# Kernel tuning notes

Hardware: AMD Instinct MI355X
Metric: run time of the kernel (lower is better)

The kernel has to match this reference:

```python
import jax, jax.numpy as jnp
import numpy as np

CNT_R = 500
DIM = 128
B, NEI = 8192, 64


def setup_inputs() -> dict:
    key = jax.random.key(0)
    ks = jax.random.split(key, 10)
    d2 = 2 * DIM
    return {
        "batch_nei_e_emb": jax.random.normal(ks[0], (B, NEI, DIM), dtype=jnp.float32),
        "batch_nei_rw": jax.random.uniform(ks[1], (B, NEI), dtype=jnp.float32),
        "w_r_table": jax.random.normal(ks[2], (2 * CNT_R + 1, DIM), dtype=jnp.float32),
        "zq_table": jax.random.normal(ks[3], (2 * CNT_R, DIM), dtype=jnp.float32),
        "attn_W_w": jax.random.normal(ks[4], (d2, d2), dtype=jnp.float32) / np.sqrt(d2),
        "attn_W_b": jnp.zeros((d2,), dtype=jnp.float32),
        "u_a_w": jax.random.normal(ks[5], (d2,), dtype=jnp.float32) / np.sqrt(d2),
        "u_a_b": jnp.zeros((), dtype=jnp.float32),
        "batch_nei_rid": jax.random.randint(ks[6], (B, NEI), 0, 2 * CNT_R + 1),
        "batch_q_rid": jax.random.randint(ks[7], (B,), 0, 2 * CNT_R),
    }


def reference(batch_nei_e_emb, batch_nei_rw, w_r_table, zq_table,
              attn_W_w, attn_W_b, u_a_w, u_a_b,
              batch_nei_rid, batch_q_rid):
    # gather relation hyperplane normals: (B, NEI, DIM)
    w_r = w_r_table[batch_nei_rid]
    n = w_r / jnp.linalg.norm(w_r, axis=-1, keepdims=True)
    # hyperplane projection: e - (e . n) n
    e = batch_nei_e_emb
    e_proj = e - jnp.sum(e * n, axis=-1, keepdims=True) * n
    # query relation embedding, tiled over neighbors: (B, NEI, DIM)
    z_q = zq_table[batch_q_rid]  # (B, DIM)
    z_q = jnp.broadcast_to(z_q[:, None, :], e_proj.shape)
    concat = jnp.concatenate([z_q, e_proj], axis=-1)  # (B, NEI, 2*DIM)
    h = jnp.tanh(jnp.einsum('bni,oi->bno', concat, attn_W_w) + attn_W_b)
    _alpha = jnp.einsum('bni,i->bn', h, u_a_w) + u_a_b  # (B, NEI)
    alpha = jax.nn.softmax(_alpha, axis=-1)
    attn = alpha + batch_nei_rw
    return attn
```

## Files before the change

### kernel.cpp

```cpp
#include <hip/hip_runtime.h>

#define NB    8192
#define NEI   64
#define DIM   128
#define D2    256
#define NR_W  1001
#define NR_Z  1000
#define EPB_LD 136

typedef __attribute__((ext_vector_type(8))) short bf16x8;
typedef __attribute__((ext_vector_type(4))) float f32x4;

__device__ __forceinline__ ushort f2bf(float x) {
    union { float f; unsigned u; } c; c.f = x;
    unsigned u = c.u;
    return (ushort)((u + 0x7fffu + ((u >> 16) & 1u)) >> 16);
}


__global__ void k_norm(const float* __restrict__ w_r_table, float* __restrict__ norm_t) {
    int r = blockIdx.x;
    int t = threadIdx.x;
    float v = w_r_table[r * DIM + t];
    float s = v * v;
    #pragma unroll
    for (int m = 1; m < 64; m <<= 1) s += __shfl_xor(s, m);
    __shared__ float sh[2];
    if ((t & 63) == 0) sh[t >> 6] = s;
    __syncthreads();
    float tot = sh[0] + sh[1];
    norm_t[r * DIM + t] = v / sqrtf(tot);
}

__global__ void k_tq(const float* __restrict__ zq_table, const float* __restrict__ W,
                     const float* __restrict__ bias, float* __restrict__ tq_t) {
    int r = blockIdx.x;
    int o = threadIdx.x;
    __shared__ float4 z4[32];
    if (o < 32) z4[o] = ((const float4*)(zq_table + r * DIM))[o];
    __syncthreads();
    const float4* wr = (const float4*)(W + o * D2);
    float acc = bias[o];
    #pragma unroll 8
    for (int i = 0; i < 32; ++i) {
        float4 wv = wr[i], zv = z4[i];
        acc += wv.x*zv.x + wv.y*zv.y + wv.z*zv.z + wv.w*zv.w;
    }
    tq_t[r * D2 + o] = acc;
}

__global__ void k_bfrag(const float* __restrict__ W, ushort* __restrict__ bfrag) {
    int nt = blockIdx.x;
    int kt = blockIdx.y;
    int l  = threadIdx.x;
    int o  = nt * 16 + (l & 15);
    int k  = kt * 32 + (l >> 4) * 8;
    const float4* src = (const float4*)(W + o * D2 + DIM + k);
    float4 a = src[0], c = src[1];
    uint4 w;
    w.x = f2bf(a.x) | ((unsigned)f2bf(a.y) << 16);
    w.y = f2bf(a.z) | ((unsigned)f2bf(a.w) << 16);
    w.z = f2bf(c.x) | ((unsigned)f2bf(c.y) << 16);
    w.w = f2bf(c.z) | ((unsigned)f2bf(c.w) << 16);
    *(uint4*)(bfrag + ((nt * 4 + kt) * 64 + l) * 8) = w;
}


__global__ __launch_bounds__(256, 2) void k_main(
    const float* __restrict__ e_emb,
    const float* __restrict__ rw,
    const int*   __restrict__ nei_rid,
    const int*   __restrict__ q_rid,
    const float* __restrict__ norm_t,
    const float* __restrict__ tq_t,
    const ushort* __restrict__ bfrag,
    const float* __restrict__ u_a_w,
    float* __restrict__ out)
{
    __shared__ ushort ep16[NEI * EPB_LD];
    __shared__ float  alpw[4][NEI];

    const int b = blockIdx.x;
    const int t = threadIdx.x;
    const int wave = t >> 6, lane = t & 63;
    const int ln = lane & 15, hi = lane >> 4;

    {
        const int row = t >> 2, q = t & 3;
        const float4* esrc = (const float4*)(e_emb + ((size_t)b * NEI + row) * DIM + q * 32);
        const int rid = nei_rid[b * NEI + row];
        const float4* nsrc = (const float4*)(norm_t + rid * DIM + q * 32);
        float4 ev[8], nv[8];
        #pragma unroll
        for (int i = 0; i < 8; ++i) { ev[i] = esrc[i]; nv[i] = nsrc[i]; }
        float part = 0.f;
        #pragma unroll
        for (int i = 0; i < 8; ++i)
            part += ev[i].x*nv[i].x + ev[i].y*nv[i].y + ev[i].z*nv[i].z + ev[i].w*nv[i].w;
        part += __shfl_xor(part, 1);
        part += __shfl_xor(part, 2);
        const float d = part;
        ushort* dst = &ep16[row * EPB_LD + q * 32];
        #pragma unroll
        for (int g = 0; g < 4; ++g) {
            float4 lo = ev[g*2], hi4 = ev[g*2+1];
            float4 nl = nv[g*2], nh  = nv[g*2+1];
            lo.x = fmaf(-d, nl.x, lo.x); lo.y = fmaf(-d, nl.y, lo.y);
            lo.z = fmaf(-d, nl.z, lo.z); lo.w = fmaf(-d, nl.w, lo.w);
            hi4.x = fmaf(-d, nh.x, hi4.x); hi4.y = fmaf(-d, nh.y, hi4.y);
            hi4.z = fmaf(-d, nh.z, hi4.z); hi4.w = fmaf(-d, nh.w, hi4.w);
            uint4 w;
            w.x = f2bf(lo.x)  | ((unsigned)f2bf(lo.y)  << 16);
            w.y = f2bf(lo.z)  | ((unsigned)f2bf(lo.w)  << 16);
            w.z = f2bf(hi4.x) | ((unsigned)f2bf(hi4.y) << 16);
            w.w = f2bf(hi4.z) | ((unsigned)f2bf(hi4.w) << 16);
            *(uint4*)(dst + g * 8) = w;
        }
    }

    const int qr = q_rid[b];
    float tq4[4], ua4[4];
    #pragma unroll
    for (int nt = 0; nt < 4; ++nt) {
        int o = wave * 64 + nt * 16 + ln;
        tq4[nt] = tq_t[qr * D2 + o];
        ua4[nt] = u_a_w[o];
    }

    bf16x8 bfr_[4][4];
    #pragma unroll
    for (int nt = 0; nt < 4; ++nt)
        #pragma unroll
        for (int kt = 0; kt < 4; ++kt)
            bfr_[nt][kt] = *(const bf16x8*)(bfrag + (((wave*4 + nt)*4 + kt)*64 + lane)*8);

    __syncthreads();

    #pragma unroll
    for (int mt = 0; mt < 4; ++mt) {
        bf16x8 a_[4];
        #pragma unroll
        for (int kt = 0; kt < 4; ++kt)
            a_[kt] = *(const bf16x8*)&ep16[(mt*16 + ln) * EPB_LD + kt*32 + hi*8];
        f32x4 acc[4];
        #pragma unroll
        for (int nt = 0; nt < 4; ++nt) acc[nt] = (f32x4){0.f, 0.f, 0.f, 0.f};
        #pragma unroll
        for (int kt = 0; kt < 4; ++kt)
            #pragma unroll
            for (int nt = 0; nt < 4; ++nt)
                acc[nt] = __builtin_amdgcn_mfma_f32_16x16x32_bf16(a_[kt], bfr_[nt][kt], acc[nt], 0, 0, 0);
        float pr[4] = {0.f, 0.f, 0.f, 0.f};
        #pragma unroll
        for (int nt = 0; nt < 4; ++nt)
            #pragma unroll
            for (int j = 0; j < 4; ++j) {
                float v = acc[nt][j] + tq4[nt];
                float e2 = __expf(2.f * v);
                float r  = __builtin_amdgcn_rcpf(e2 + 1.f);
                float h  = fmaf(-2.f, r, 1.f);
                pr[j] += ua4[nt] * h;
            }
        #pragma unroll
        for (int m = 1; m < 16; m <<= 1)
            #pragma unroll
            for (int j = 0; j < 4; ++j) pr[j] += __shfl_xor(pr[j], m);
        if (ln == 0) {
            #pragma unroll
            for (int j = 0; j < 4; ++j) alpw[wave][mt*16 + hi*4 + j] = pr[j];
        }
    }
    __syncthreads();

    if (t < NEI) {
        float a = alpw[0][t] + alpw[1][t] + alpw[2][t] + alpw[3][t];
        float p = __expf(a);
        float s = p;
        #pragma unroll
        for (int m = 1; m < 64; m <<= 1) s += __shfl_xor(s, m);
        out[(size_t)b * NEI + t] = fmaf(p, __builtin_amdgcn_rcpf(s), rw[(size_t)b * NEI + t]);
    }
}


extern "C" void kernel_launch(void* const* d_in, const int* in_sizes, int n_in,
                              void* d_out, int out_size, void* d_ws, size_t ws_size,
                              hipStream_t stream) {
    const float* e_emb   = (const float*)d_in[0];
    const float* rw      = (const float*)d_in[1];
    const float* w_r_tab = (const float*)d_in[2];
    const float* zq_tab  = (const float*)d_in[3];
    const float* attn_W  = (const float*)d_in[4];
    const float* attn_b  = (const float*)d_in[5];
    const float* u_a_w   = (const float*)d_in[6];
    const int*   nei_rid = (const int*)d_in[8];
    const int*   q_rid   = (const int*)d_in[9];
    float* out = (float*)d_out;

    float* ws = (float*)d_ws;
    float* norm_t = ws;
    float* tq_t   = norm_t + NR_W * DIM;
    ushort* bfrag = (ushort*)(tq_t + NR_Z * D2);

    k_norm<<<NR_W, DIM, 0, stream>>>(w_r_tab, norm_t);
    k_tq<<<NR_Z, D2, 0, stream>>>(zq_tab, attn_W, attn_b, tq_t);
    k_bfrag<<<dim3(16, 4), 64, 0, stream>>>(attn_W, bfrag);
    k_main<<<NB, 256, 0, stream>>>(e_emb, rw, nei_rid, q_rid,
                                   norm_t, tq_t, bfrag, u_a_w, out);
}
```

Baseline: 126.9 us.

## Make main kernel persistent over 16 batches with async LDS prefetch of embeddings

Each workgroup now runs 512 threads and loops over 16 batch rows. The next row's embedding tile is prefetched straight into LDS with global_load_lds, and its rid/rw/tq values are loaded into registers while the current row computes. B fragments are loaded once per block and split across 8 waves. The tanh is rewritten algebraically as 1-2/(1+exp2) with the u_a sum precomputed, which saves a multiply per element. This aims to hide HBM latency and amortise setup, at the cost of more LDS, an extra barrier per row and fewer blocks (512).

```diff
diff --git a/kernel.cpp b/kernel.cpp
--- a/kernel.cpp
+++ b/kernel.cpp
@@ -1,4 +1,5 @@
 #include <hip/hip_runtime.h>
+#include <hip/hip_bf16.h>
 
 #define NB    8192
 #define NEI   64
@@ -7,6 +8,8 @@
 #define NR_W  1001
 #define NR_Z  1000
 #define EPB_LD 136
+#define BPB   16
+#define C2L2E 2.8853900817779268f
 
 typedef __attribute__((ext_vector_type(8))) short bf16x8;
 typedef __attribute__((ext_vector_type(4))) float f32x4;
@@ -15,6 +18,17 @@
     union { float f; unsigned u; } c; c.f = x;
     unsigned u = c.u;
     return (ushort)((u + 0x7fffu + ((u >> 16) & 1u)) >> 16);
+}
+
+__device__ __forceinline__ unsigned pk2(float a, float b) {
+    __hip_bfloat162 h = __float22bfloat162_rn(make_float2(a, b));
+    return *(unsigned*)&h;
+}
+
+__device__ __forceinline__ void gll16(const void* g, void* l) {
+    __builtin_amdgcn_global_load_lds(
+        (const __attribute__((address_space(1))) unsigned int*)g,
+        (__attribute__((address_space(3))) unsigned int*)l, 16, 0, 0);
 }
 
 
@@ -50,10 +64,10 @@
 }
 
 __global__ void k_bfrag(const float* __restrict__ W, ushort* __restrict__ bfrag) {
-    int nt = blockIdx.x;
+    int ot = blockIdx.x;
     int kt = blockIdx.y;
     int l  = threadIdx.x;
-    int o  = nt * 16 + (l & 15);
+    int o  = ot * 16 + (l & 15);
     int k  = kt * 32 + (l >> 4) * 8;
     const float4* src = (const float4*)(W + o * D2 + DIM + k);
     float4 a = src[0], c = src[1];
@@ -62,11 +76,22 @@
     w.y = f2bf(a.z) | ((unsigned)f2bf(a.w) << 16);
     w.z = f2bf(c.x) | ((unsigned)f2bf(c.y) << 16);
     w.w = f2bf(c.z) | ((unsigned)f2bf(c.w) << 16);
-    *(uint4*)(bfrag + ((nt * 4 + kt) * 64 + l) * 8) = w;
-}
-
-
-__global__ __launch_bounds__(256, 2) void k_main(
+    *(uint4*)(bfrag + ((ot * 4 + kt) * 64 + l) * 8) = w;
+}
+
+__global__ void k_sua(const float* __restrict__ u, float* __restrict__ sua) {
+    int t = threadIdx.x;
+    float v = u[t];
+    #pragma unroll
+    for (int m = 1; m < 64; m <<= 1) v += __shfl_xor(v, m);
+    __shared__ float sh[4];
+    if ((t & 63) == 0) sh[t >> 6] = v;
+    __syncthreads();
+    if (t == 0) sua[0] = sh[0] + sh[1] + sh[2] + sh[3];
+}
+
+
+__global__ __launch_bounds__(512, 4) void k_main(
     const float* __restrict__ e_emb,
     const float* __restrict__ rw,
     const int*   __restrict__ nei_rid,
@@ -74,111 +99,167 @@
     const float* __restrict__ norm_t,
     const float* __restrict__ tq_t,
     const ushort* __restrict__ bfrag,
+    const float* __restrict__ u_a_sum,
     const float* __restrict__ u_a_w,
     float* __restrict__ out)
 {
-    __shared__ ushort ep16[NEI * EPB_LD];
-    __shared__ float  alpw[4][NEI];
-
-    const int b = blockIdx.x;
-    const int t = threadIdx.x;
+    __shared__ __align__(16) float  e_raw[NEI * DIM];
+    __shared__ __align__(16) ushort ep16[NEI * EPB_LD];
+    __shared__ float alpw[8][NEI];
+
+    const int t    = threadIdx.x;
     const int wave = t >> 6, lane = t & 63;
-    const int ln = lane & 15, hi = lane >> 4;
-
-    {
-        const int row = t >> 2, q = t & 3;
-        const float4* esrc = (const float4*)(e_emb + ((size_t)b * NEI + row) * DIM + q * 32);
-        const int rid = nei_rid[b * NEI + row];
-        const float4* nsrc = (const float4*)(norm_t + rid * DIM + q * 32);
-        float4 ev[8], nv[8];
-        #pragma unroll
-        for (int i = 0; i < 8; ++i) { ev[i] = esrc[i]; nv[i] = nsrc[i]; }
-        float part = 0.f;
-        #pragma unroll
-        for (int i = 0; i < 8; ++i)
-            part += ev[i].x*nv[i].x + ev[i].y*nv[i].y + ev[i].z*nv[i].z + ev[i].w*nv[i].w;
-        part += __shfl_xor(part, 1);
-        part += __shfl_xor(part, 2);
-        const float d = part;
-        ushort* dst = &ep16[row * EPB_LD + q * 32];
-        #pragma unroll
-        for (int g = 0; g < 4; ++g) {
-            float4 lo = ev[g*2], hi4 = ev[g*2+1];
-            float4 nl = nv[g*2], nh  = nv[g*2+1];
-            lo.x = fmaf(-d, nl.x, lo.x); lo.y = fmaf(-d, nl.y, lo.y);
-            lo.z = fmaf(-d, nl.z, lo.z); lo.w = fmaf(-d, nl.w, lo.w);
-            hi4.x = fmaf(-d, nh.x, hi4.x); hi4.y = fmaf(-d, nh.y, hi4.y);
-            hi4.z = fmaf(-d, nh.z, hi4.z); hi4.w = fmaf(-d, nh.w, hi4.w);
-            uint4 w;
-            w.x = f2bf(lo.x)  | ((unsigned)f2bf(lo.y)  << 16);
-            w.y = f2bf(lo.z)  | ((unsigned)f2bf(lo.w)  << 16);
-            w.z = f2bf(hi4.x) | ((unsigned)f2bf(hi4.y) << 16);
-            w.w = f2bf(hi4.z) | ((unsigned)f2bf(hi4.w) << 16);
-            *(uint4*)(dst + g * 8) = w;
-        }
-    }
-
-    const int qr = q_rid[b];
-    float tq4[4], ua4[4];
-    #pragma unroll
-    for (int nt = 0; nt < 4; ++nt) {
-        int o = wave * 64 + nt * 16 + ln;
-        tq4[nt] = tq_t[qr * D2 + o];
-        ua4[nt] = u_a_w[o];
-    }
-
-    bf16x8 bfr_[4][4];
-    #pragma unroll
-    for (int nt = 0; nt < 4; ++nt)
+    const int ln   = lane & 15, hi = lane >> 4;
+    const int row  = t >> 3, q3 = t & 7;
+    const int b0   = blockIdx.x * BPB;
+
+    bf16x8 bfr_[2][4];
+    #pragma unroll
+    for (int nt = 0; nt < 2; ++nt)
         #pragma unroll
         for (int kt = 0; kt < 4; ++kt)
-            bfr_[nt][kt] = *(const bf16x8*)(bfrag + (((wave*4 + nt)*4 + kt)*64 + lane)*8);
-
-    __syncthreads();
-
-    #pragma unroll
-    for (int mt = 0; mt < 4; ++mt) {
-        bf16x8 a_[4];
+            bfr_[nt][kt] = *(const bf16x8*)(bfrag + ((((wave*2+nt)*4 + kt)*64 + lane)*8));
+    asm volatile("" : "+v"(bfr_[0][0]), "+v"(bfr_[0][1]), "+v"(bfr_[0][2]), "+v"(bfr_[0][3]),
+                      "+v"(bfr_[1][0]), "+v"(bfr_[1][1]), "+v"(bfr_[1][2]), "+v"(bfr_[1][3]));
+
+    float ua2[2];
+    #pragma unroll
+    for (int nt = 0; nt < 2; ++nt) ua2[nt] = u_a_w[wave*32 + nt*16 + ln];
+    asm volatile("" : "+v"(ua2[0]), "+v"(ua2[1]));
+    const float sua = u_a_sum[0];
+
+    unsigned soff[4];
+    #pragma unroll
+    for (int c = 0; c < 4; ++c) {
+        unsigned D = (unsigned)(wave*4096 + c*1024 + lane*16);
+        unsigned r7 = (unsigned)((wave*8 + 2*c + (lane>>5)) & 7);
+        soff[c] = D ^ (r7 << 4);
+    }
+    const char* ebase = (const char*)e_emb;
+
+    #pragma unroll
+    for (int c = 0; c < 4; ++c)
+        gll16(ebase + (((size_t)b0) << 15) + soff[c], (char*)e_raw + wave*4096 + c*1024);
+    int   rid_c = nei_rid[b0 * NEI + row];
+    float rw_c  = rw[(size_t)b0 * NEI + (t & 63)];
+    float tqc[2];
+    {
+        int qr = q_rid[b0];
         #pragma unroll
-        for (int kt = 0; kt < 4; ++kt)
-            a_[kt] = *(const bf16x8*)&ep16[(mt*16 + ln) * EPB_LD + kt*32 + hi*8];
-        f32x4 acc[4];
+        for (int nt = 0; nt < 2; ++nt)
+            tqc[nt] = C2L2E * tq_t[qr * D2 + wave*32 + nt*16 + ln];
+    }
+    int   rid_n = 0;  float rw_n = 0.f;  float tqn[2] = {0.f, 0.f};
+
+    __syncthreads();
+
+    #pragma unroll 1
+    for (int i = 0; i < BPB; ++i) {
+        const int b = b0 + i;
+
+        {
+            const float4* nsrc = (const float4*)(norm_t + rid_c * DIM + q3 * 16);
+            float4 nv[4];
+            #pragma unroll
+            for (int k = 0; k < 4; ++k) nv[k] = nsrc[k];
+            const unsigned rbase = (unsigned)(row * 512 + q3 * 64);
+            const unsigned rx = (unsigned)((row & 7) << 4);
+            float4 ev[4];
+            #pragma unroll
+            for (int k = 0; k < 4; ++k)
+                ev[k] = *(const float4*)((const char*)e_raw + ((rbase + k*16) ^ rx));
+            float part = 0.f;
+            #pragma unroll
+            for (int k = 0; k < 4; ++k)
+                part += ev[k].x*nv[k].x + ev[k].y*nv[k].y + ev[k].z*nv[k].z + ev[k].w*nv[k].w;
+            part += __shfl_xor(part, 1);
+            part += __shfl_xor(part, 2);
+            part += __shfl_xor(part, 4);
+            const float d = part;
+            float p0 = fmaf(-d, nv[0].x, ev[0].x), p1 = fmaf(-d, nv[0].y, ev[0].y);
+            float p2 = fmaf(-d, nv[0].z, ev[0].z), p3 = fmaf(-d, nv[0].w, ev[0].w);
+            float p4 = fmaf(-d, nv[1].x, ev[1].x), p5 = fmaf(-d, nv[1].y, ev[1].y);
+            float p6 = fmaf(-d, nv[1].z, ev[1].z), p7 = fmaf(-d, nv[1].w, ev[1].w);
+            uint4 w0; w0.x = pk2(p0,p1); w0.y = pk2(p2,p3); w0.z = pk2(p4,p5); w0.w = pk2(p6,p7);
+            float s0 = fmaf(-d, nv[2].x, ev[2].x), s1 = fmaf(-d, nv[2].y, ev[2].y);
+            float s2 = fmaf(-d, nv[2].z, ev[2].z), s3 = fmaf(-d, nv[2].w, ev[2].w);
+            float s4 = fmaf(-d, nv[3].x, ev[3].x), s5 = fmaf(-d, nv[3].y, ev[3].y);
+            float s6 = fmaf(-d, nv[3].z, ev[3].z), s7 = fmaf(-d, nv[3].w, ev[3].w);
+            uint4 w1; w1.x = pk2(s0,s1); w1.y = pk2(s2,s3); w1.z = pk2(s4,s5); w1.w = pk2(s6,s7);
+            char* dst = (char*)ep16 + row * (EPB_LD*2) + q3 * 32;
+            *(uint4*)dst = w0;
+            *(uint4*)(dst + 16) = w1;
+        }
+
+        __syncthreads();
+
+        if (i + 1 < BPB) {
+            const size_t ebo = ((size_t)(b + 1)) << 15;
+            #pragma unroll
+            for (int c = 0; c < 4; ++c)
+                gll16(ebase + ebo + soff[c], (char*)e_raw + wave*4096 + c*1024);
+            rid_n = nei_rid[(b + 1) * NEI + row];
+            rw_n  = rw[(size_t)(b + 1) * NEI + (t & 63)];
+            int qr1 = q_rid[b + 1];
+            #pragma unroll
+            for (int nt = 0; nt < 2; ++nt)
+                tqn[nt] = tq_t[qr1 * D2 + wave*32 + nt*16 + ln];
+        }
+
         #pragma unroll
-        for (int nt = 0; nt < 4; ++nt) acc[nt] = (f32x4){0.f, 0.f, 0.f, 0.f};
-        #pragma unroll
-        for (int kt = 0; kt < 4; ++kt)
-            #pragma unroll
-            for (int nt = 0; nt < 4; ++nt)
-                acc[nt] = __builtin_amdgcn_mfma_f32_16x16x32_bf16(a_[kt], bfr_[nt][kt], acc[nt], 0, 0, 0);
-        float pr[4] = {0.f, 0.f, 0.f, 0.f};
-        #pragma unroll
-        for (int nt = 0; nt < 4; ++nt)
-            #pragma unroll
-            for (int j = 0; j < 4; ++j) {
-                float v = acc[nt][j] + tq4[nt];
-                float e2 = __expf(2.f * v);
-                float r  = __builtin_amdgcn_rcpf(e2 + 1.f);
-                float h  = fmaf(-2.f, r, 1.f);
-                pr[j] += ua4[nt] * h;
+        for (int mt = 0; mt < 4; ++mt) {
+            bf16x8 a_[4];
+            #pragma unroll
+            for (int kt = 0; kt < 4; ++kt)
+                a_[kt] = *(const bf16x8*)&ep16[(mt*16 + ln) * EPB_LD + kt*32 + hi*8];
+            f32x4 acc[2];
+            #pragma unroll
+            for (int nt = 0; nt < 2; ++nt) acc[nt] = (f32x4){0.f, 0.f, 0.f, 0.f};
+            #pragma unroll
+            for (int kt = 0; kt < 4; ++kt)
+                #pragma unroll
+                for (int nt = 0; nt < 2; ++nt)
+                    acc[nt] = __builtin_amdgcn_mfma_f32_16x16x32_bf16(a_[kt], bfr_[nt][kt], acc[nt], 0, 0, 0);
+            float pr[4] = {0.f, 0.f, 0.f, 0.f};
+            #pragma unroll
+            for (int nt = 0; nt < 2; ++nt)
+                #pragma unroll
+                for (int j = 0; j < 4; ++j) {
+                    float e2 = __builtin_exp2f(fmaf(C2L2E, acc[nt][j], tqc[nt]));
+                    float r  = __builtin_amdgcn_rcpf(e2 + 1.f);
+                    pr[j] = fmaf(ua2[nt], r, pr[j]);
+                }
+            #pragma unroll
+            for (int m = 1; m < 16; m <<= 1)
+                #pragma unroll
+                for (int j = 0; j < 4; ++j) pr[j] += __shfl_xor(pr[j], m);
+            if (ln == 0) {
+                #pragma unroll
+                for (int j = 0; j < 4; ++j) alpw[wave][mt*16 + hi*4 + j] = pr[j];
             }
-        #pragma unroll
-        for (int m = 1; m < 16; m <<= 1)
-            #pragma unroll
-            for (int j = 0; j < 4; ++j) pr[j] += __shfl_xor(pr[j], m);
-        if (ln == 0) {
-            #pragma unroll
-            for (int j = 0; j < 4; ++j) alpw[wave][mt*16 + hi*4 + j] = pr[j];
-        }
-    }
-    __syncthreads();
-
-    if (t < NEI) {
-        float a = alpw[0][t] + alpw[1][t] + alpw[2][t] + alpw[3][t];
-        float p = __expf(a);
-        float s = p;
-        #pragma unroll
-        for (int m = 1; m < 64; m <<= 1) s += __shfl_xor(s, m);
-        out[(size_t)b * NEI + t] = fmaf(p, __builtin_amdgcn_rcpf(s), rw[(size_t)b * NEI + t]);
+        }
+
+        __syncthreads();
+
+        if (t < NEI) {
+            float s8 = 0.f;
+            #pragma unroll
+            for (int w = 0; w < 8; ++w) s8 += alpw[w][t];
+            float a = fmaf(-2.f, s8, sua);
+            float p = __expf(a);
+            float s = p;
+            #pragma unroll
+            for (int m = 1; m < 64; m <<= 1) s += __shfl_xor(s, m);
+            out[(size_t)b * NEI + t] = fmaf(p, __builtin_amdgcn_rcpf(s), rw_c);
+        }
+
+        if (i + 1 < BPB) {
+            rid_c = rid_n;
+            rw_c  = rw_n;
+            tqc[0] = C2L2E * tqn[0];
+            tqc[1] = C2L2E * tqn[1];
+            asm volatile("" : "+v"(rid_c), "+v"(rw_c), "+v"(tqc[0]), "+v"(tqc[1]));
+        }
     }
 }
 
@@ -201,10 +282,12 @@
     float* norm_t = ws;
     float* tq_t   = norm_t + NR_W * DIM;
     ushort* bfrag = (ushort*)(tq_t + NR_Z * D2);
+    float* suap   = (float*)(bfrag + 16*4*64*8);
 
     k_norm<<<NR_W, DIM, 0, stream>>>(w_r_tab, norm_t);
     k_tq<<<NR_Z, D2, 0, stream>>>(zq_tab, attn_W, attn_b, tq_t);
     k_bfrag<<<dim3(16, 4), 64, 0, stream>>>(attn_W, bfrag);
-    k_main<<<NB, 256, 0, stream>>>(e_emb, rw, nei_rid, q_rid,
-                                   norm_t, tq_t, bfrag, u_a_w, out);
-}
+    k_sua<<<1, 256, 0, stream>>>(u_a_w, suap);
+    k_main<<<NB / BPB, 512, 0, stream>>>(e_emb, rw, nei_rid, q_rid,
+                                         norm_t, tq_t, bfrag, suap, u_a_w, out);
+}
```

Measured after the change: 151.2 us. 19.2% more time.
